# Kernel optimization log

Hardware: AMD Instinct MI355X
Metric: run time of the kernel (lower is better)

## Reference

```python
import jax, jax.numpy as jnp
import numpy as np

B = 32
NUM_CLASSES = 2


def _conv3d(x, w, b):
    # 3x3x3 'same' conv, NCDHW
    y = jax.lax.conv_general_dilated(x, w, (1, 1, 1), [(1, 1)] * 3,
                                     dimension_numbers=("NCDHW", "OIDHW", "NCDHW"))
    return y + b[None, :, None, None, None]


def _bn(x, g, b, axes, eps=1e-5):
    # training-mode batchnorm (biased variance), channel axis = 1
    m = jnp.mean(x, axes, keepdims=True)
    v = jnp.var(x, axes, keepdims=True)
    sh = [1] * x.ndim
    sh[1] = -1
    return (x - m) / jnp.sqrt(v + eps) * g.reshape(sh) + b.reshape(sh)


def _ln(x, g, b, eps=1e-6):
    m = jnp.mean(x, -1, keepdims=True)
    v = jnp.var(x, -1, keepdims=True)
    return (x - m) / jnp.sqrt(v + eps) * g + b


def _lin(x, w, b):
    return x @ w.T + b


def _conv1x1(x, w, b):
    # 1x1x1 Conv3d == channel-mixing linear
    return jnp.einsum("bcdhw,oc->bodhw", x, w) + b[None, :, None, None, None]


def _catnum(t, w, b, g, be, attr, out_attr):
    # Conv1d(attr->196, k=1) == Linear; BN1d over (batch, length); SiLU; tile channels
    t = _lin(t.reshape(t.shape[0], attr), w, b)               # [B,196]
    t = _bn(t[:, :, None], g, be, (0, 2))[:, :, 0]
    t = t * jax.nn.sigmoid(t)                                  # SiLU
    return jnp.broadcast_to(t.reshape(-1, 1, 4, 7, 7), (t.shape[0], out_attr, 4, 7, 7))


def _gcn(t, w, b):
    # all-pairs L1-distance affinity over CHANNELS (detached), then matmul + MLP + residual
    bsz, c = t.shape[0], t.shape[1]
    f = t.reshape(bsz, c, -1)                                  # [B,C,196]
    dist = jax.lax.stop_gradient(
        jnp.exp(-jnp.abs(f[:, :, None, :] - f[:, None, :, :]).sum(-1)))  # [B,C,C]
    out = jax.nn.relu(_lin(jnp.einsum("bij,bjn->bin", dist, f), w, b))
    return out.reshape(t.shape) + t


def _crossatt(img, text, e1_w, e1_b, e2_w, e2_b, f1_w, f1_b, f2_w, f2_b, f3_w, f3_b, f4_w, f4_b):
    # q/k/v each come from the SAME linear applied to the same input -> identical tensors
    iq = jax.nn.relu(_lin(img, e1_w, e1_b))                    # [B,128,196]
    tq = jax.nn.relu(_lin(text, e2_w, e2_b))                   # [B,45,196]
    att = lambda q, k: jax.nn.softmax(jnp.einsum("bik,bjk->bij", q, k), axis=-1)
    img_fea = att(iq, iq) @ iq
    text_fea = att(tq, tq) @ tq
    it_fea = att(iq, tq) @ tq
    ti_fea = att(tq, iq) @ iq
    return (_lin(img_fea, f1_w, f1_b) + _lin(it_fea, f3_w, f3_b) + img,
            _lin(text_fea, f2_w, f2_b) + _lin(ti_fea, f4_w, f4_b) + text)


def _cmsa(xf, w, b, fw, fb):
    # query=key=value (same conv applied thrice to same input)
    bsz, c, d, hh, ww = xf.shape
    q = jax.nn.relu(_conv1x1(xf, w, b)).reshape(bsz, c, -1)    # [B,173,196]
    A = jax.nn.softmax(jnp.einsum("bci,bcj->bij", q, q), axis=-1)  # [B,196,196]
    fea = jnp.einsum("bij,bcj->bci", A, q).reshape(bsz, c, d, hh, ww)
    return jax.nn.relu(_conv1x1(fea, fw, fb)) + xf


def _forward(x, oneHot, num, c1_w1, c1_b1, c1_g1, c1_be1, c1_w2, c1_b2, c1_g2, c1_be2,
             oh_w, oh_b, oh_g, oh_be, nm_w, nm_b, nm_g, nm_be,
             gm1_w, gm1_b, gm2_w, gm2_b, ln1_g, ln1_b, ln2_g, ln2_b,
             e1_w, e1_b, e2_w, e2_b, f1_w, f1_b, f2_w, f2_b, f3_w, f3_b, f4_w, f4_b,
             cm_w, cm_b, cmf_w, cmf_b, cls_w, cls_b):
    h = jax.nn.relu(_bn(_conv3d(x, c1_w1, c1_b1), c1_g1, c1_be1, (0, 2, 3, 4)))
    conv5 = jax.nn.relu(_bn(_conv3d(h, c1_w2, c1_b2), c1_g2, c1_be2, (0, 2, 3, 4)))  # [B,128,4,7,7]
    t_oh = _catnum(oneHot, oh_w, oh_b, oh_g, oh_be, 24, 30)    # [B,30,4,7,7]
    t_nm = _catnum(num, nm_w, nm_b, nm_g, nm_be, 11, 15)       # [B,15,4,7,7]
    text = jnp.concatenate([t_oh, t_nm], axis=1)               # [B,45,4,7,7]
    conv5 = _gcn(conv5, gm1_w, gm1_b)
    text = _gcn(text, gm2_w, gm2_b)
    bsz = x.shape[0]
    c5f = conv5.reshape(bsz, 128, 196)
    txf = text.reshape(bsz, 45, 196)
    ci, ct = _crossatt(_ln(c5f, ln1_g, ln1_b), _ln(txf, ln2_g, ln2_b),
                       e1_w, e1_b, e2_w, e2_b, f1_w, f1_b, f2_w, f2_b, f3_w, f3_b, f4_w, f4_b)
    feat = jnp.concatenate([(ci + c5f).reshape(bsz, 128, 4, 7, 7),
                            (ct + txf).reshape(bsz, 45, 4, 7, 7)], axis=1)  # [B,173,4,7,7]
    cmsa = _cmsa(feat, cm_w, cm_b, cmf_w, cmf_b)
    g1v = t_oh.reshape(bsz, 30, -1).sum(-1)
    g2v = t_nm.reshape(bsz, 15, -1).sum(-1)
    pcm = cmsa.reshape(bsz, 173, -1).sum(-1)
    return _lin(jnp.concatenate([g1v, g2v, pcm], axis=1), cls_w, cls_b)  # [B,num_classes]


def setup_inputs():
    key = jax.random.key(0)
    ks = iter(jax.random.split(key, 64))
    rn = lambda shape, s=0.02: jax.random.normal(next(ks), shape, jnp.float32) * s
    d = {}
    d["x"] = rn((B, 320, 4, 7, 7), 1.0)
    d["oneHot"] = (jax.random.uniform(next(ks), (B, 24)) > 0.5).astype(jnp.float32)
    d["num"] = rn((B, 11), 1.0)
    d["c1_w1"] = rn((128, 320, 3, 3, 3)); d["c1_b1"] = jnp.zeros(128)
    d["c1_g1"] = jnp.ones(128); d["c1_be1"] = jnp.zeros(128)
    d["c1_w2"] = rn((128, 128, 3, 3, 3)); d["c1_b2"] = jnp.zeros(128)
    d["c1_g2"] = jnp.ones(128); d["c1_be2"] = jnp.zeros(128)
    d["oh_w"] = rn((196, 24), 0.1); d["oh_b"] = jnp.zeros(196)
    d["oh_g"] = jnp.ones(196); d["oh_be"] = jnp.zeros(196)
    d["nm_w"] = rn((196, 11), 0.1); d["nm_b"] = jnp.zeros(196)
    d["nm_g"] = jnp.ones(196); d["nm_be"] = jnp.zeros(196)
    d["gm1_w"] = rn((196, 196), 0.05); d["gm1_b"] = jnp.zeros(196)
    d["gm2_w"] = rn((196, 196), 0.05); d["gm2_b"] = jnp.zeros(196)
    d["ln1_g"] = jnp.ones(196); d["ln1_b"] = jnp.zeros(196)
    d["ln2_g"] = jnp.ones(196); d["ln2_b"] = jnp.zeros(196)
    for n in ["e1", "e2", "f1", "f2", "f3", "f4"]:
        d[n + "_w"] = rn((196, 196), 0.05); d[n + "_b"] = jnp.zeros(196)
    d["cm_w"] = rn((173, 173), 0.05); d["cm_b"] = jnp.zeros(173)
    d["cmf_w"] = rn((173, 173), 0.05); d["cmf_b"] = jnp.zeros(173)
    d["cls_w"] = rn((NUM_CLASSES, 218), 0.05); d["cls_b"] = jnp.zeros(NUM_CLASSES)
    return d


def reference(x, oneHot, num, c1_w1, c1_b1, c1_g1, c1_be1, c1_w2, c1_b2, c1_g2, c1_be2,
              oh_w, oh_b, oh_g, oh_be, nm_w, nm_b, nm_g, nm_be,
              gm1_w, gm1_b, gm2_w, gm2_b, ln1_g, ln1_b, ln2_g, ln2_b,
              e1_w, e1_b, e2_w, e2_b, f1_w, f1_b, f2_w, f2_b, f3_w, f3_b, f4_w, f4_b,
              cm_w, cm_b, cmf_w, cmf_b, cls_w, cls_b):
    return _forward(x, oneHot, num, c1_w1, c1_b1, c1_g1, c1_be1, c1_w2, c1_b2, c1_g2, c1_be2,
                    oh_w, oh_b, oh_g, oh_be, nm_w, nm_b, nm_g, nm_be,
                    gm1_w, gm1_b, gm2_w, gm2_b, ln1_g, ln1_b, ln2_g, ln2_b,
                    e1_w, e1_b, e2_w, e2_b, f1_w, f1_b, f2_w, f2_b, f3_w, f3_b, f4_w, f4_b,
                    cm_w, cm_b, cmf_w, cmf_b, cls_w, cls_b)
```

## Files before the change

kernel.cpp:

```cpp
#include <hip/hip_runtime.h>
#include <hip/hip_bf16.h>


using bf16x8 = __attribute__((ext_vector_type(8))) short;
using f32x4  = __attribute__((ext_vector_type(4))) float;

typedef const __attribute__((address_space(1))) void gas_void;
typedef __attribute__((address_space(3))) void las_void;

__device__ __forceinline__ unsigned short f2bf(float f) {
    unsigned int u = __float_as_uint(f);
    u += 0x7FFFu + ((u >> 16) & 1u);
    return (unsigned short)(u >> 16);
}

__device__ __forceinline__ void d_wpack(const float* __restrict__ w,
                                        unsigned short* __restrict__ wp,
                                        int IC, int idx) {
    int nc = IC >> 3;
    if (idx >= 27 * 128 * nc) return;
    int c = idx % nc; int r = idx / nc; int oc = r & 127; int t = r >> 7;
    const float* ws = w + ((size_t)oc * IC + c * 8) * 27 + t;
    unsigned int o0 = f2bf(ws[0])   | ((unsigned int)f2bf(ws[27])  << 16);
    unsigned int o1 = f2bf(ws[54])  | ((unsigned int)f2bf(ws[81])  << 16);
    unsigned int o2 = f2bf(ws[108]) | ((unsigned int)f2bf(ws[135]) << 16);
    unsigned int o3 = f2bf(ws[162]) | ((unsigned int)f2bf(ws[189]) << 16);
    uint4 v; v.x = o0; v.y = o1; v.z = o2; v.w = o3;
    ((uint4*)wp)[idx] = v;
}

__device__ __forceinline__ void d_w173(const float* __restrict__ w,
                                       unsigned short* __restrict__ wb, int idx) {
    if (idx >= 176 * 192) return;
    int oc = idx / 192, c = idx - oc * 192;
    wb[idx] = (oc < 173 && c < 173) ? f2bf(w[(size_t)oc * 173 + c]) : (unsigned short)0;
}

__device__ __forceinline__ void d_wcat(const float* __restrict__ wA,
                                       const float* __restrict__ wB,
                                       unsigned short* __restrict__ outw, int idx) {
    if (idx >= 208 * 448) return;
    int n = idx / 448, k = idx - n * 448;
    unsigned short v = 0;
    if (n < 196) {
        if (k < 196) v = f2bf(wA[(size_t)n * 196 + k]);
        else if (k >= 224 && k < 420) v = f2bf(wB[(size_t)n * 196 + (k - 224)]);
    }
    outw[idx] = v;
}

__device__ __forceinline__ void d_catnum(const float* __restrict__ inp, int A,
                                         const float* __restrict__ w,
                                         const float* __restrict__ bias,
                                         const float* __restrict__ g,
                                         const float* __restrict__ be,
                                         float* __restrict__ outv, int j, int lane) {
    float v = 0.f;
    if (lane < 32) {
        v = bias[j];
        for (int k = 0; k < A; ++k) v += inp[lane * A + k] * w[j * A + k];
    }
    float s = (lane < 32) ? v : 0.f;
    float s2 = (lane < 32) ? v * v : 0.f;
    for (int m = 16; m; m >>= 1) { s += __shfl_xor(s, m, 32); s2 += __shfl_xor(s2, m, 32); }
    if (lane < 32) {
        float mean = s / 32.f;
        float var = s2 / 32.f - mean * mean;
        float rstd = rsqrtf(var + 1e-5f);
        float t = (v - mean) * rstd * g[j] + be[j];
        t = t / (1.f + expf(-t));
        outv[lane * 196 + j] = t;
    }
}

__global__ void k_prep1(const float* __restrict__ c1w1, unsigned short* __restrict__ wp1,
                        const float* __restrict__ c1w2, unsigned short* __restrict__ wp2,
                        const float* __restrict__ x, unsigned short* __restrict__ xt1) {
    int blk = blockIdx.x, tid = threadIdx.x;
    if (blk < 540) { d_wpack(c1w1, wp1, 320, blk * 256 + tid); return; }
    blk -= 540;
    if (blk < 216) { d_wpack(c1w2, wp2, 128, blk * 256 + tid); return; }
    blk -= 216;
    int b = blk / 147, ib = blk - b * 147;
    const int tot = 5 * 208 * 36;
    int idx = ib * 256 + tid;
    if (idx >= tot) return;
    int g = idx / (208 * 36); int r2 = idx - g * (208 * 36);
    int s = r2 / 36, cp = r2 - s * 36;
    int cc = cp * 2;
    int ic = g * 64 + cc;
    unsigned int lo = 0, hi = 0;
    if (s < 196 && cc < 64 && ic < 320)         lo = f2bf(x[((size_t)b * 320 + ic) * 196 + s]);
    if (s < 196 && cc + 1 < 64 && ic + 1 < 320) hi = f2bf(x[((size_t)b * 320 + ic + 1) * 196 + s]);
    ((unsigned int*)xt1)[(size_t)b * tot + idx] = lo | (hi << 16);
}

__global__ void k_prep2(const float* __restrict__ cm_w, unsigned short* __restrict__ wcmb,
                        const float* __restrict__ cmf_w, unsigned short* __restrict__ wcmfb,
                        const float* __restrict__ gm1_w, unsigned short* __restrict__ gm1b,
                        float4* __restrict__ ftbz,
                        const float* __restrict__ gm2_w, const float* __restrict__ e1_w,
                        const float* __restrict__ e2_w, float* __restrict__ wT) {
    int blk = blockIdx.x, tid = threadIdx.x;
    if (blk < 132) { d_w173(cm_w, wcmb, blk * 256 + tid); return; }
    blk -= 132;
    if (blk < 132) { d_w173(cmf_w, wcmfb, blk * 256 + tid); return; }
    blk -= 132;
    if (blk < 182) {
        int idx = blk * 256 + tid;
        if (idx < 208 * 224) {
            int r = idx / 224, c = idx - r * 224;
            gm1b[idx] = (r < 196 && c < 196) ? f2bf(gm1_w[(size_t)r * 196 + c])
                                             : (unsigned short)0;
        }
        return;
    }
    blk -= 182;
    if (blk < 624) {
        int i = blk * 256 + tid;
        if (i < 159744) ftbz[i] = (float4){0.f, 0.f, 0.f, 0.f};
        return;
    }
    blk -= 624;
    {
        int m = blk / 196, i = blk - m * 196;
        const float* w = (m == 0) ? gm2_w : (m == 1) ? e1_w : e2_w;
        float* o = wT + (size_t)m * 38416;
        if (tid < 196) o[(size_t)i * 196 + tid] = w[(size_t)tid * 196 + i];
    }
}

__global__ void k_catnum2(const float* __restrict__ oneHot, const float* __restrict__ num,
                          const float* __restrict__ ohw, const float* __restrict__ ohb,
                          const float* __restrict__ ohg, const float* __restrict__ ohbe,
                          const float* __restrict__ nmw, const float* __restrict__ nmb,
                          const float* __restrict__ nmg, const float* __restrict__ nmbe,
                          float* __restrict__ toh, float* __restrict__ tnm) {
    int blk = blockIdx.x;
    if (blk < 196) d_catnum(oneHot, 24, ohw, ohb, ohg, ohbe, toh, blk, threadIdx.x);
    else           d_catnum(num, 11, nmw, nmb, nmg, nmbe, tnm, blk - 196, threadIdx.x);
}

__device__ __forceinline__ void d_dist_img(const float* __restrict__ f,
                                           const float* __restrict__ fT,
                                           unsigned short* __restrict__ distb,
                                           int bx, int b, int tid) {
    __shared__ float fi[4][196];
    const int i0 = bx * 4;
    for (int idx = tid; idx < 4 * 196; idx += 256) {
        int r = idx / 196, n = idx - r * 196;
        fi[r][n] = f[((size_t)(b * 128 + i0 + r)) * 196 + n];
    }
    __syncthreads();
    if (tid < 128) {
        const float* ft = fT + (size_t)b * 196 * 128 + tid;
        float a[4];
#pragma unroll
        for (int r = 0; r < 4; ++r) a[r] = 0.f;
#pragma unroll 4
        for (int n = 0; n < 196; ++n) {
            float v = ft[(size_t)n * 128];
#pragma unroll
            for (int r = 0; r < 4; ++r) a[r] += fabsf(fi[r][n] - v);
        }
#pragma unroll
        for (int r = 0; r < 4; ++r)
            distb[((size_t)(b * 128 + i0 + r)) * 128 + tid] = f2bf(expf(-a[r]));
    }
}

__device__ __forceinline__ void d_dist_txt(const float* __restrict__ f,
                                           const float* __restrict__ fT,
                                           float* __restrict__ dist,
// ... 327 lines not shown
                    int col = nt * 16 + a;
                    p0[((size_t)b * 208 + row) * 224 + col] = f2bf(e[nt] * inv);
                }
            }
        }
    } else if (EPI == 2) {
#pragma unroll
        for (int nt = 0; nt < 13; ++nt) {
            if (nt < NT0 || nt >= NT0 + NTN) continue;
            int col = nt * 16 + a;
#pragma unroll
            for (int j = 0; j < 4; ++j) {
                int row = mbase + j;
                if (row < 173)
                    p0[((size_t)b * 208 + col) * 192 + row] = f2bf(acc[nt][j]);
            }
        }
    } else if (EPI == 3) {
#pragma unroll
        for (int nt = 0; nt < 13; ++nt) {
            if (nt < NT0 || nt >= NT0 + NTN) continue;
            int col = nt * 16 + a;
            if (col < 196) {
#pragma unroll
                for (int j = 0; j < 4; ++j) {
                    int row = mbase + j;
                    if (row < 173) {
                        size_t rr = ((size_t)b * 173 + row) * 196 + col;
                        outf[rr] = fmaxf(acc[nt][j] + bias[row], 0.f) + resid[rr];
                    }
                }
            }
        }
    } else if (EPI == 7) {
#pragma unroll
        for (int nt = 0; nt < 13; ++nt) {
            if (nt < NT0 || nt >= NT0 + NTN) continue;
            int col = nt * 16 + a;
#pragma unroll
            for (int j = 0; j < 4; ++j) {
                int row = mbase + j;
                unsigned short h = (col < 196) ? f2bf(acc[nt][j]) : (unsigned short)0;
                p0[((size_t)b * 128 + row) * 224 + col] = h;
            }
        }
    } else {
#pragma unroll
        for (int nt = 0; nt < 13; ++nt) {
            if (nt < NT0 || nt >= NT0 + NTN) continue;
            int col = nt * 16 + a;
            if (col < 196) {
#pragma unroll
                for (int j = 0; j < 4; ++j) {
                    int row = mbase + j;
                    size_t rr = ((size_t)b * 128 + row) * 196 + col;
                    outf[rr] = fmaxf(acc[nt][j] + bias[col], 0.f) + resid[rr];
                }
            }
        }
    }
}

template <int MROWS, int MTILES, int KPA, int KPB, int KK, int EPI, int STAGEA, int NS>
__global__ __launch_bounds__(256, 2) void k_agemm(
    const unsigned short* __restrict__ Ab, size_t ABS,
    const unsigned short* __restrict__ Bb, size_t BBS,
    const float* __restrict__ biasA, const float* __restrict__ biasB,
    const float* __restrict__ lnres, const float* __restrict__ res2,
    unsigned short* __restrict__ p0, size_t p0rs, size_t p0bs,
    float* __restrict__ feat, unsigned short* __restrict__ ftb, int cbase) {
    constexpr int KPS = KPA + 8;
    __shared__ unsigned short xsA[STAGEA ? 64 * KPS : 64];
    __shared__ char bbuf[2][208 * 64];
    const int tid = threadIdx.x, bx = blockIdx.x, b = blockIdx.y;
    const int wv = tid >> 6, lane = tid & 63, a = lane & 15, kg = lane >> 4;
    const int nh = bx % NS, mg = bx / NS;
    const int NT0 = (NS == 1) ? 0 : nh * 7;
    const int NTN = (NS == 1) ? 13 : ((nh == 0) ? 7 : 6);

    const unsigned short* Abase = Ab + (size_t)b * ABS;
    if (STAGEA) {
        const int rowu = KPA / 2;
        for (int i = tid; i < 64 * rowu; i += 256) {
            int r = i / rowu, cu = i - r * rowu;
            int gr = mg * 64 + r; if (gr > MROWS - 1) gr = MROWS - 1;
            unsigned int v = ((const unsigned int*)(Abase + (size_t)gr * KPA))[cu];
            *(unsigned int*)&xsA[r * KPS + cu * 2] = v;
        }
    }
    const char* Bbase = (const char*)(Bb + (size_t)b * BBS);
    auto stageB = [&](int kk) {
        char* dst0 = &bbuf[kk & 1][0];
        const int cnt = NTN * 64;
#pragma unroll
        for (int c = 0; c < 4; ++c) {
            int idx = tid + c * 256;
            if (idx < cnt) {
                int lrow = idx >> 2, u = idx & 3;
                int grow = NT0 * 16 + lrow;
                gas_void* src = (gas_void*)(Bbase + (size_t)grow * (KPB * 2) +
                                            kk * 64 + u * 16);
                __builtin_amdgcn_global_load_lds(src, (las_void*)(dst0 + (size_t)idx * 16),
                                                 16, 0, 0);
            }
        }
    };

    int mt = mg * 4 + wv; if (mt > MTILES - 1) mt = MTILES - 1;

    f32x4 acc[13];
#pragma unroll
    for (int nt = 0; nt < 13; ++nt) acc[nt] = (f32x4){0.f, 0.f, 0.f, 0.f};

    stageB(0);
    __syncthreads();
    for (int kk = 0; kk < KK; ++kk) {
        if (kk + 1 < KK) stageB(kk + 1);
        bf16x8 Af;
        if (STAGEA) {
            int arow = mt * 16 + a - mg * 64;
            Af = *(const bf16x8*)&xsA[arow * KPS + kk * 32 + kg * 8];
        } else {
            int gr = mt * 16 + a; if (gr > MROWS - 1) gr = MROWS - 1;
// ... 19 lines not shown
#pragma unroll
            for (int nt = 0; nt < 8; ++nt) mA = fmaxf(mA, acc[nt][j]);
#pragma unroll
            for (int nt = 8; nt < 13; ++nt) {
                int col = nt * 16 + a;
                float s = (col < 173) ? acc[nt][j] : -3.4e38f;
                mB = fmaxf(mB, s);
            }
            for (int msk = 1; msk < 16; msk <<= 1) {
                mA = fmaxf(mA, __shfl_xor(mA, msk));
                mB = fmaxf(mB, __shfl_xor(mB, msk));
            }
            float eA[8], eB[5];
            float sA = 0.f, sB = 0.f;
#pragma unroll
            for (int nt = 0; nt < 8; ++nt) { eA[nt] = expf(acc[nt][j] - mA); sA += eA[nt]; }
#pragma unroll
            for (int nt = 8; nt < 13; ++nt) {
                int col = nt * 16 + a;
                float v = (col < 173) ? expf(acc[nt][j] - mB) : 0.f;
                eB[nt - 8] = v; sB += v;
            }
            for (int msk = 1; msk < 16; msk <<= 1) {
                sA += __shfl_xor(sA, msk);
                sB += __shfl_xor(sB, msk);
            }
            float iA = 1.f / sA, iB = 1.f / sB;
            if (row < MROWS) {
#pragma unroll
                for (int nt = 0; nt < 12; ++nt) {
                    int col = nt * 16 + a;
                    float v = (nt < 8) ? eA[nt] * iA
                                       : ((col < 173) ? eB[nt - 8] * iB : 0.f);
                    p0[(size_t)b * p0bs + (size_t)row * p0rs + col] = f2bf(v);
                }
            }
        }
    } else {
#pragma unroll
        for (int nt = 0; nt < 13; ++nt) {
            if (nt < NT0 || nt >= NT0 + NTN) continue;
            int col = nt * 16 + a;
            if (col < 196) {
#pragma unroll
                for (int j = 0; j < 4; ++j) {
                    int row = mbase + j;
                    if (row < MROWS) {
                        size_t rr = ((size_t)b * MROWS + row) * 196 + col;
                        float v = acc[nt][j] + biasA[col] + biasB[col] +
                                  lnres[rr] + res2[rr];
                        feat[((size_t)b * 173 + cbase + row) * 196 + col] = v;
                        ftb[((size_t)(b * 208 + col)) * 192 + cbase + row] = f2bf(v);
                    }
                }
            }
        }
    }
}

template <int MROWS, int MTILES, int NS>
__global__ __launch_bounds__(256, 2) void k_pv(
    const unsigned short* __restrict__ P, size_t Pbs,
    const unsigned short* __restrict__ V1, size_t V1bs,
    const unsigned short* __restrict__ V2, size_t V2bs,
    unsigned short* __restrict__ F, size_t Fbs) {
    constexpr int KPS = 200;
    __shared__ unsigned short xsA[64 * KPS];
    __shared__ char bbuf[2][208 * 64];
    const int tid = threadIdx.x, bx = blockIdx.x, b = blockIdx.y;
    const int wv = tid >> 6, lane = tid & 63, a = lane & 15, kg = lane >> 4;
    const int nh = bx % NS, mg = bx / NS;
    const int NT0 = (NS == 1) ? 0 : nh * 7;
    const int NTN = (NS == 1) ? 13 : ((nh == 0) ? 7 : 6);

    const unsigned short* Abase = P + (size_t)b * Pbs;
    {
        for (int i = tid; i < 64 * 96; i += 256) {
            int r = i / 96, cu = i - r * 96;
            int gr = mg * 64 + r; if (gr > MROWS - 1) gr = MROWS - 1;
            unsigned int v = ((const unsigned int*)(Abase + (size_t)gr * 192))[cu];
            *(unsigned int*)&xsA[r * KPS + cu * 2] = v;
        }
    }
    int mt = mg * 4 + wv; if (mt > MTILES - 1) mt = MTILES - 1;
    const int arow = mt * 16 + a - mg * 64;
    const int mbase = mt * 16 + kg * 4;

    auto run = [&](const unsigned short* Vb, size_t Vbs_, int KPB, int KK,
                   int AOFFe, int outoff) {
        f32x4 acc[13];
#pragma unroll
        for (int nt = 0; nt < 13; ++nt) acc[nt] = (f32x4){0.f, 0.f, 0.f, 0.f};
        const char* Bbase = (const char*)(Vb + (size_t)b * Vbs_);
        auto stageB = [&](int kk) {
            char* dst0 = &bbuf[kk & 1][0];
            const int cnt = NTN * 64;
#pragma unroll
            for (int c = 0; c < 4; ++c) {
                int idx = tid + c * 256;
                if (idx < cnt) {
                    int lrow = idx >> 2, u = idx & 3;
                    int grow = NT0 * 16 + lrow;
                    gas_void* src = (gas_void*)(Bbase + (size_t)grow * (KPB * 2) +
                                                kk * 64 + u * 16);
                    __builtin_amdgcn_global_load_lds(src,
                        (las_void*)(dst0 + (size_t)idx * 16), 16, 0, 0);
                }
            }
        };
        stageB(0);
        __syncthreads();
        for (int kk = 0; kk < KK; ++kk) {
            if (kk + 1 < KK) stageB(kk + 1);
            bf16x8 Af = *(const bf16x8*)&xsA[arow * KPS + AOFFe + kk * 32 + kg * 8];
            const char* bb = &bbuf[kk & 1][0];
#pragma unroll
            for (int nt = 0; nt < 13; ++nt) {
                if (nt >= NT0 && nt < NT0 + NTN) {
                    bf16x8 Bf = *(const bf16x8*)(bb + ((nt - NT0) * 16 + a) * 64 + kg * 16);
                    acc[nt] = __builtin_amdgcn_mfma_f32_16x16x32_bf16(Af, Bf, acc[nt], 0, 0, 0);
                }
            }
            __syncthreads();
        }
#pragma unroll
        for (int nt = 0; nt < 13; ++nt) {
            if (nt < NT0 || nt >= NT0 + NTN) continue;
            int col = nt * 16 + a;
#pragma unroll
            for (int j = 0; j < 4; ++j) {
                int row = mbase + j;
                if (row < MROWS) {
                    unsigned short h = (col < 196) ? f2bf(acc[nt][j]) : (unsigned short)0;
                    F[(size_t)b * Fbs + (size_t)row * 448 + outoff + col] = h;
                }
            }
        }
        if (nh == NS - 1) {
            int col = 208 + a;
#pragma unroll
            for (int j = 0; j < 4; ++j) {
                int row = mbase + j;
                if (row < MROWS)
                    F[(size_t)b * Fbs + (size_t)row * 448 + outoff + col] = 0;
            }
        }
    };
    run(V1, V1bs, 128, 4, 0, 0);
    run(V2, V2bs, 64, 2, 128, 224);
}

template <int C, int ROWS>
__global__ void k_gcn_spmmfin_t(const float* __restrict__ dist, const float* __restrict__ f,
                                const float* __restrict__ wt, const float* __restrict__ bias,
                                float* __restrict__ outp) {
    __shared__ float ds[ROWS][C];
    __shared__ float ts[ROWS][196];
    const int i0 = blockIdx.x * ROWS, b = blockIdx.y;
    const int tid = threadIdx.x;
    for (int idx = tid; idx < ROWS * C; idx += 256) {
        int r = idx / C, j = idx - r * C;
        ds[r][j] = dist[((size_t)(b * C + i0 + r)) * C + j];
    }
    __syncthreads();
    if (tid < 196) {
        float a[ROWS];
#pragma unroll
        for (int r = 0; r < ROWS; ++r) a[r] = 0.f;
#pragma unroll 4
        for (int j = 0; j < C; ++j) {
            float v = f[((size_t)b * C + j) * 196 + tid];
#pragma unroll
            for (int r = 0; r < ROWS; ++r) a[r] += ds[r][j] * v;
        }
#pragma unroll
        for (int r = 0; r < ROWS; ++r) ts[r][tid] = a[r];
    }
    __syncthreads();
    if (tid < 196) {
        float a[ROWS];
        float bi = bias[tid];
#pragma unroll
        for (int r = 0; r < ROWS; ++r) a[r] = bi;
#pragma unroll 4
        for (int n = 0; n < 196; ++n) {
            float wv = wt[(size_t)n * 196 + tid];
#pragma unroll
            for (int r = 0; r < ROWS; ++r) a[r] += ts[r][n] * wv;
        }
#pragma unroll
        for (int r = 0; r < ROWS; ++r) {
            size_t rr = ((size_t)(b * C + i0 + r)) * 196 + tid;
            outp[rr] = fmaxf(a[r], 0.f) + f[rr];
        }
    }
}

__global__ void k_textbuild(const float* __restrict__ toh, const float* __restrict__ tnm,
                            float* __restrict__ text, float* __restrict__ textT) {
    int idx = blockIdx.x;
    int b = idx / 45, c = idx - b * 45;
    int s = threadIdx.x;
    if (s < 196) {
        float v = (c < 30) ? toh[b * 196 + s] : tnm[b * 196 + s];
        text[(size_t)idx * 196 + s] = v;
        textT[((size_t)b * 196 + s) * 45 + c] = v;
    }
}

template <int R, int ROWS, int KOFF, int TS>
__device__ __forceinline__ void d_lnlin(const float* __restrict__ x,
                                        const float* __restrict__ g,
                                        const float* __restrict__ be,
                                        const float* __restrict__ eT,
                                        const float* __restrict__ eb,
                                        float* __restrict__ lnout,
                                        unsigned short* __restrict__ kcat,
                                        unsigned short* __restrict__ tbuf,
                                        int bx, int b) {
    __shared__ float ls[ROWS][196];
    const int i0 = bx * ROWS;
    const int tid = threadIdx.x;
    const int wv = tid >> 6, lane = tid & 63;
    for (int idx = tid; idx < ROWS * 196; idx += 256) {
        int r = idx / 196, n = idx - r * 196;
        ls[r][n] = x[((size_t)(b * R + i0 + r)) * 196 + n];
    }
    __syncthreads();
    for (int k = 0;; ++k) {
        int r = wv + 4 * k;
        if (r >= ROWS) break;
        float s = 0.f, s2 = 0.f;
        for (int j = lane; j < 196; j += 64) { float v = ls[r][j]; s += v; s2 += v * v; }
        for (int sh = 32; sh; sh >>= 1) { s += __shfl_xor(s, sh); s2 += __shfl_xor(s2, sh); }
        float mean = s / 196.f;
        float var = s2 / 196.f - mean * mean;
        float rstd = rsqrtf(var + 1e-6f);
        size_t rowo = ((size_t)(b * R + i0 + r)) * 196;
        for (int j = lane; j < 196; j += 64) {
            float l = (ls[r][j] - mean) * rstd * g[j] + be[j];
// ... 102 lines not shown
    const float* gm2_w  = (const float*)d_in[21];
    const float* gm2_b  = (const float*)d_in[22];
    const float* ln1_g  = (const float*)d_in[23];
    const float* ln1_b  = (const float*)d_in[24];
    const float* ln2_g  = (const float*)d_in[25];
    const float* ln2_b  = (const float*)d_in[26];
    const float* e1_w   = (const float*)d_in[27];
    const float* e1_b   = (const float*)d_in[28];
    const float* e2_w   = (const float*)d_in[29];
    const float* e2_b   = (const float*)d_in[30];
    const float* f1_w   = (const float*)d_in[31];
    const float* f1_b   = (const float*)d_in[32];
    const float* f2_w   = (const float*)d_in[33];
    const float* f2_b   = (const float*)d_in[34];
    const float* f3_w   = (const float*)d_in[35];
    const float* f3_b   = (const float*)d_in[36];
    const float* f4_w   = (const float*)d_in[37];
    const float* f4_b   = (const float*)d_in[38];
    const float* cm_w   = (const float*)d_in[39];
    const float* cm_b   = (const float*)d_in[40];
    const float* cmf_w  = (const float*)d_in[41];
    const float* cmf_b  = (const float*)d_in[42];
    const float* cls_w  = (const float*)d_in[43];
    const float* cls_b  = (const float*)d_in[44];
    float* out = (float*)d_out;
    float* W = (float*)d_ws;

    const size_t L = 802816;
    const size_t T = 282240;
    const size_t F3 = 1085056;
    const size_t o_A    = 0;
    const size_t o_B    = L;
    const size_t o_C    = 2 * L;
    const size_t o_part = 3 * L;
    const size_t o_Kcat = 3 * L;
    const size_t o_iqT  = o_Kcat + 745472;
    const size_t o_t1   = 4 * L + T;
    const size_t o_t3   = 4 * L + 2 * T;
    const size_t o_ln2  = 4 * L + 3 * T;
    const size_t o_toh  = 4 * L + 4 * T;
    const size_t o_tnm  = o_toh + 6272;
    const size_t o_st   = o_tnm + 6272;
    const size_t o_wT   = o_st + 1024;
    const size_t o_feat = o_wT + 8 * 38416;
    const size_t o_q    = o_feat + F3;
    const size_t o_Fimg = o_q;
    const size_t o_dd   = o_q + F3;
    const size_t o_db   = o_dd;
    const size_t o_d2   = o_dd + 524288;
    const size_t o_gm1b = o_dd + 589088;
    const size_t o_fTb  = o_dd + 612384;
    const size_t o_tqT  = o_dd;
    const size_t o_wcI  = o_dd + 212992;
    const size_t o_wcT  = o_wcI + 46592;
    const size_t o_pbf  = o_dd;
    const size_t o_rs   = o_dd;
    const size_t o_qbf  = o_dd + 745472;
    const size_t o_Ftxt = o_qbf;
    const size_t o_wcm  = o_qbf + 630784;
    const size_t o_wcmf = o_wcm + 16896;
    const size_t o_ftb  = o_wcmf + 16896;
    const size_t o_tr   = o_ftb + 638976;
    const size_t o_Pimg = o_tr;
    const size_t o_Ptxt = o_tr + 393216;
    const size_t o_qtb  = o_tr;
    const size_t o_feab = o_qtb + 638976;
    const size_t o_ps   = 10158208;
    const size_t o_xt1 = o_dd;
    const size_t o_xt2 = o_xt1 + 1198080;
    const size_t o_wp1 = o_xt2 + 479232;
    const size_t o_wp2 = o_wp1 + 552960;

    float* part = W + o_part;
    unsigned short* xt1 = (unsigned short*)(W + o_xt1);
    unsigned short* xt2 = (unsigned short*)(W + o_xt2);
    unsigned short* wp1 = (unsigned short*)(W + o_wp1);
    unsigned short* wp2 = (unsigned short*)(W + o_wp2);
    unsigned short* kcatb = (unsigned short*)(W + o_Kcat);
    unsigned short* iqTb = (unsigned short*)(W + o_iqT);
    unsigned short* tqTb = (unsigned short*)(W + o_tqT);
    unsigned short* wcatI = (unsigned short*)(W + o_wcI);
    unsigned short* wcatT = (unsigned short*)(W + o_wcT);
    unsigned short* Fimg = (unsigned short*)(W + o_Fimg);
    unsigned short* Ftxt = (unsigned short*)(W + o_Ftxt);
    unsigned short* Pimg = (unsigned short*)(W + o_Pimg);
    unsigned short* Ptxt = (unsigned short*)(W + o_Ptxt);
    unsigned short* ftb = (unsigned short*)(W + o_ftb);
    unsigned short* qtb = (unsigned short*)(W + o_qtb);
    unsigned short* feab = (unsigned short*)(W + o_feab);
    unsigned short* qbf = (unsigned short*)(W + o_qbf);
    unsigned short* wcmb = (unsigned short*)(W + o_wcm);
    unsigned short* wcmfb = (unsigned short*)(W + o_wcmf);
    unsigned short* pbf = (unsigned short*)(W + o_pbf);
    unsigned short* distb = (unsigned short*)(W + o_db);
    unsigned short* gm1b = (unsigned short*)(W + o_gm1b);
    unsigned short* fTb = (unsigned short*)(W + o_fTb);
    unsigned short* tmpb = (unsigned short*)(W + o_A);
    float* gm2T = W + o_wT + 0 * 38416;
    float* e1T  = W + o_wT + 1 * 38416;
    float* e2T  = W + o_wT + 2 * 38416;

    k_prep1<<<5460, 256, 0, stream>>>(c1_w1, wp1, c1_w2, wp2, x, xt1);

    k_convchunk4<320, 5, 4, 2><<<dim3(20, 32), 256, 0, stream>>>(xt1, wp1, part);
    k_reduce_stats<5, 128><<<dim3(128, 32), 256, 0, stream>>>(part, W + o_A, W + o_ps);
    k_bn_apply2<<<4096, 256, 0, stream>>>(W + o_A, W + o_ps, c1_g1, c1_be1,
                                          nullptr, nullptr, xt2, 128);

    k_convchunk4<128, 2, 2, 4><<<dim3(16, 32), 256, 0, stream>>>(xt2, wp2, part);
    k_reduce_stats<2, 128><<<dim3(128, 32), 256, 0, stream>>>(part, W + o_B,
                                                              W + o_ps + 8192);
    k_bn_apply2<<<4096, 256, 0, stream>>>(W + o_B, W + o_ps + 8192, c1_g2, c1_be2,
                                          W + o_tr, fTb, nullptr, 128);

    k_prep2<<<1658, 256, 0, stream>>>(cm_w, wcmb, cmf_w, wcmfb, gm1_w, gm1b,
                                      (float4*)(W + o_ftb), gm2_w, e1_w, e2_w, W + o_wT);

    k_catnum2<<<392, 64, 0, stream>>>(oneHot, num, oh_w, oh_b, oh_g, oh_be,
                                      nm_w, nm_b, nm_g, nm_be, W + o_toh, W + o_tnm);
    k_textbuild<<<32 * 45, 256, 0, stream>>>(W + o_toh, W + o_tnm, W + o_t1, W + o_tr + L);

    k_dist_both<<<1504, 256, 0, stream>>>(W + o_B, W + o_tr, distb,
                                          W + o_t1, W + o_tr + L, W + o_d2);

    k_bgemm<128, 8, 128, 4, 7, 2><<<dim3(4, 32), 256, 0, stream>>>(
        distb, (size_t)128 * 128, fTb, (size_t)208 * 128, nullptr,
        tmpb, nullptr, nullptr, nullptr);
    k_bgemm<128, 8, 224, 7, 8, 2><<<dim3(4, 32), 256, 0, stream>>>(
        tmpb, (size_t)128 * 224, gm1b, 0, gm1_b,
        nullptr, nullptr, W + o_B, W + o_C);

    k_gcn_spmmfin_t<45, 3><<<dim3(15, 32), 256, 0, stream>>>(W + o_d2, W + o_t1, gm2T,
                                                             gm2_b, W + o_t3);

    k_prep3<<<936, 256, 0, stream>>>((float4*)(W + o_tqT), f1_w, f3_w, wcatI,
                                     f4_w, f2_w, wcatT);

    k_lnlin_both<<<1504, 256, 0, stream>>>(W + o_C, ln1_g, ln1_b, e1T, e1_b, W + o_B,
                                           W + o_t3, ln2_g, ln2_b, e2T, e2_b, W + o_ln2,
                                           kcatb, iqTb, tqTb);

    k_agemm<128, 8, 224, 224, 7, 5, 1, 1><<<dim3(2, 32), 256, 0, stream>>>(
        kcatb, (size_t)208 * 224, kcatb, (size_t)208 * 224,
        nullptr, nullptr, nullptr, nullptr, Pimg, 192, (size_t)128 * 192,
        nullptr, nullptr, 0);
    k_agemm<45, 3, 224, 224, 7, 5, 1, 1><<<dim3(1, 32), 256, 0, stream>>>(
        kcatb + 128 * 224, (size_t)208 * 224, kcatb, (size_t)208 * 224,
        nullptr, nullptr, nullptr, nullptr, Ptxt, 192, (size_t)48 * 192,
        nullptr, nullptr, 0);

    k_pv<128, 8, 2><<<dim3(4, 32), 256, 0, stream>>>(
        Pimg, (size_t)128 * 192, iqTb, (size_t)208 * 128, tqTb, (size_t)208 * 64,
        Fimg, (size_t)128 * 448);
    k_pv<45, 3, 2><<<dim3(2, 32), 256, 0, stream>>>(
        Ptxt, (size_t)48 * 192, iqTb, (size_t)208 * 128, tqTb, (size_t)208 * 64,
        Ftxt, (size_t)48 * 448);

    k_agemm<128, 8, 448, 448, 14, 4, 0, 2><<<dim3(4, 32), 256, 0, stream>>>(
        Fimg, (size_t)128 * 448, wcatI, 0,
        f1_b, f3_b, W + o_B, W + o_C, nullptr, 0, 0, W + o_feat, ftb, 0);
    k_agemm<45, 3, 448, 448, 14, 4, 0, 2><<<dim3(2, 32), 256, 0, stream>>>(
        Ftxt, (size_t)48 * 448, wcatT, 0,
        f2_b, f4_b, W + o_ln2, W + o_t3, nullptr, 0, 0, W + o_feat, ftb, 128);

    k_prep4<<<2592, 256, 0, stream>>>((float4*)(W + o_pbf), (float4*)(W + o_qtb));

    k_bgemm<176, 11, 192, 6, 0, 2><<<dim3(6, 32), 256, 0, stream>>>(
        wcmb, 0, ftb, (size_t)208 * 192, cm_b, qbf, qtb, nullptr, nullptr);
    k_bgemm<208, 13, 192, 6, 1, 1><<<dim3(4, 32), 256, 0, stream>>>(
        qtb, (size_t)208 * 192, qtb, (size_t)208 * 192, nullptr, pbf, nullptr,
        nullptr, nullptr);
    k_bgemm<176, 11, 224, 7, 2, 2><<<dim3(6, 32), 256, 0, stream>>>(
        qbf, (size_t)176 * 224, pbf, (size_t)208 * 224, nullptr, feab, nullptr,
        nullptr, nullptr);
    k_bgemm<176, 11, 192, 6, 3, 2><<<dim3(6, 32), 256, 0, stream>>>(
        wcmfb, 0, feab, (size_t)208 * 192, cmf_b, nullptr, nullptr,
        W + o_feat, W + o_q);

    k_finale<<<32, 256, 0, stream>>>(W + o_toh, W + o_tnm, W + o_q, cls_w, cls_b, out);
}
```

Baseline: 369.9 us.

## Merge paired image/text kernels into single launches to cut launch count

Several launches are merged. The catnum BN/SiLU kernel now writes the tiled text tensor and its transpose directly, removing the separate textbuild kernel. The dist×f MFMA GEMM and the text GCN spmm/MLP now run as one kernel whose blocks branch by blockIdx. The image and text attention GEMMs, PV and fusion GEMMs are each combined into one launch using parameter structs and a block split index. This removes about six launches and their serial gaps, and lets small text work share the grid with image work. The cost is some runtime parameter selection, MROWS/MTILES turned from compile-time template values into runtime values, and a larger shared-memory footprint from the union in the fused kernel.

```diff
diff --git a/kernel.cpp b/kernel.cpp
--- a/kernel.cpp
+++ b/kernel.cpp
@@ -47,30 +47,6 @@
         else if (k >= 224 && k < 420) v = f2bf(wB[(size_t)n * 196 + (k - 224)]);
     }
     outw[idx] = v;
-}
-
-__device__ __forceinline__ void d_catnum(const float* __restrict__ inp, int A,
-                                         const float* __restrict__ w,
-                                         const float* __restrict__ bias,
-                                         const float* __restrict__ g,
-                                         const float* __restrict__ be,
-                                         float* __restrict__ outv, int j, int lane) {
-    float v = 0.f;
-    if (lane < 32) {
-        v = bias[j];
-        for (int k = 0; k < A; ++k) v += inp[lane * A + k] * w[j * A + k];
-    }
-    float s = (lane < 32) ? v : 0.f;
-    float s2 = (lane < 32) ? v * v : 0.f;
-    for (int m = 16; m; m >>= 1) { s += __shfl_xor(s, m, 32); s2 += __shfl_xor(s2, m, 32); }
-    if (lane < 32) {
-        float mean = s / 32.f;
-        float var = s2 / 32.f - mean * mean;
-        float rstd = rsqrtf(var + 1e-5f);
-        float t = (v - mean) * rstd * g[j] + be[j];
-        t = t / (1.f + expf(-t));
-        outv[lane * 196 + j] = t;
-    }
 }
 
 __global__ void k_prep1(const float* __restrict__ c1w1, unsigned short* __restrict__ wp1,
@@ -130,15 +106,52 @@
     }
 }
 
-__global__ void k_catnum2(const float* __restrict__ oneHot, const float* __restrict__ num,
+__global__ void k_cattext(const float* __restrict__ oneHot, const float* __restrict__ num,
                           const float* __restrict__ ohw, const float* __restrict__ ohb,
                           const float* __restrict__ ohg, const float* __restrict__ ohbe,
                           const float* __restrict__ nmw, const float* __restrict__ nmb,
                           const float* __restrict__ nmg, const float* __restrict__ nmbe,
-                          float* __restrict__ toh, float* __restrict__ tnm) {
+                          float* __restrict__ toh, float* __restrict__ tnm,
+                          float* __restrict__ text, float* __restrict__ textT) {
     int blk = blockIdx.x;
-    if (blk < 196) d_catnum(oneHot, 24, ohw, ohb, ohg, ohbe, toh, blk, threadIdx.x);
-    else           d_catnum(num, 11, nmw, nmb, nmg, nmbe, tnm, blk - 196, threadIdx.x);
+    int lane = threadIdx.x;
+    const int isOH = (blk < 196);
+    const int j = isOH ? blk : blk - 196;
+    const float* inp = isOH ? oneHot : num;
+    const int A = isOH ? 24 : 11;
+    const float* w = isOH ? ohw : nmw;
+    const float* bias = isOH ? ohb : nmb;
+    const float* g = isOH ? ohg : nmg;
+    const float* be = isOH ? ohbe : nmbe;
+    float v = 0.f;
+    if (lane < 32) {
+        v = bias[j];
+        for (int k = 0; k < A; ++k) v += inp[lane * A + k] * w[j * A + k];
+    }
+    float s = (lane < 32) ? v : 0.f;
+    float s2 = (lane < 32) ? v * v : 0.f;
+    for (int m = 16; m; m >>= 1) { s += __shfl_xor(s, m, 32); s2 += __shfl_xor(s2, m, 32); }
+    if (lane < 32) {
+        float mean = s / 32.f;
+        float var = s2 / 32.f - mean * mean;
+        float rstd = rsqrtf(var + 1e-5f);
+        float t = (v - mean) * rstd * g[j] + be[j];
+        t = t / (1.f + expf(-t));
+        int b = lane;
+        if (isOH) {
+            toh[b * 196 + j] = t;
+            for (int c = 0; c < 30; ++c) {
+                text[((size_t)(b * 45 + c)) * 196 + j] = t;
+                textT[((size_t)(b * 196 + j)) * 45 + c] = t;
+            }
+        } else {
+            tnm[b * 196 + j] = t;
+            for (int c = 30; c < 45; ++c) {
+                text[((size_t)(b * 45 + c)) * 196 + j] = t;
+                textT[((size_t)(b * 196 + j)) * 45 + c] = t;
+            }
+        }
+    }
 }
 
 __device__ __forceinline__ void d_dist_img(const float* __restrict__ f,
@@ -532,18 +545,6 @@
                 }
             }
         }
-    } else if (EPI == 7) {
-#pragma unroll
-        for (int nt = 0; nt < 13; ++nt) {
-            if (nt < NT0 || nt >= NT0 + NTN) continue;
-            int col = nt * 16 + a;
-#pragma unroll
-            for (int j = 0; j < 4; ++j) {
-                int row = mbase + j;
-                unsigned short h = (col < 196) ? f2bf(acc[nt][j]) : (unsigned short)0;
-                p0[((size_t)b * 128 + row) * 224 + col] = h;
-            }
-        }
     } else {
 #pragma unroll
         for (int nt = 0; nt < 13; ++nt) {
@@ -561,24 +562,144 @@
     }
 }
 
-template <int MROWS, int MTILES, int KPA, int KPB, int KK, int EPI, int STAGEA, int NS>
-__global__ __launch_bounds__(256, 2) void k_agemm(
-    const unsigned short* __restrict__ Ab, size_t ABS,
-    const unsigned short* __restrict__ Bb, size_t BBS,
-    const float* __restrict__ biasA, const float* __restrict__ biasB,
-    const float* __restrict__ lnres, const float* __restrict__ res2,
-    unsigned short* __restrict__ p0, size_t p0rs, size_t p0bs,
-    float* __restrict__ feat, unsigned short* __restrict__ ftb, int cbase) {
+__global__ __launch_bounds__(256, 2) void k_gcnpair(
+    const unsigned short* __restrict__ distb, const unsigned short* __restrict__ fTb,
+    unsigned short* __restrict__ tmpb,
+    const float* __restrict__ d2, const float* __restrict__ t1,
+    const float* __restrict__ gm2T, const float* __restrict__ gm2b,
+    float* __restrict__ t3) {
+    __shared__ unsigned short xsA[64 * 136];
+    __shared__ char bbuf[2][208 * 64];
+    __shared__ float ds[3][45];
+    __shared__ float ts[3][196];
+    const int tid = threadIdx.x, b = blockIdx.y;
+    int bx = blockIdx.x;
+    if (bx < 4) {
+        const int wv = tid >> 6, lane = tid & 63, a = lane & 15, kg = lane >> 4;
+        const int nh = bx % 2, mg = bx / 2;
+        const int NT0 = nh * 7, NTN = (nh == 0) ? 7 : 6;
+        const unsigned short* Abase = distb + (size_t)b * 128 * 128;
+        for (int i = tid; i < 64 * 64; i += 256) {
+            int r = i / 64, cu = i - r * 64;
+            int gr = mg * 64 + r;
+            unsigned int v = ((const unsigned int*)(Abase + (size_t)gr * 128))[cu];
+            *(unsigned int*)&xsA[r * 136 + cu * 2] = v;
+        }
+        const char* Bbase = (const char*)(fTb + (size_t)b * 208 * 128);
+        auto stageB = [&](int kk) {
+            char* dst0 = &bbuf[kk & 1][0];
+            const int cnt = NTN * 64;
+#pragma unroll
+            for (int c = 0; c < 4; ++c) {
+                int idx = tid + c * 256;
+                if (idx < cnt) {
+                    int lrow = idx >> 2, u = idx & 3;
+                    int grow = NT0 * 16 + lrow;
+                    gas_void* src = (gas_void*)(Bbase + (size_t)grow * 256 +
+                                                kk * 64 + u * 16);
+                    __builtin_amdgcn_global_load_lds(src,
+                        (las_void*)(dst0 + (size_t)idx * 16), 16, 0, 0);
+                }
+            }
+        };
+        int mt = mg * 4 + wv;
+        const int arow = mt * 16 + a - mg * 64;
+        f32x4 acc[13];
+#pragma unroll
+        for (int nt = 0; nt < 13; ++nt) acc[nt] = (f32x4){0.f, 0.f, 0.f, 0.f};
+        stageB(0);
+        __syncthreads();
+        for (int kk = 0; kk < 4; ++kk) {
+            if (kk + 1 < 4) stageB(kk + 1);
+            bf16x8 Af = *(const bf16x8*)&xsA[arow * 136 + kk * 32 + kg * 8];
+            const char* bb = &bbuf[kk & 1][0];
+#pragma unroll
+            for (int nt = 0; nt < 13; ++nt) {
+                if (nt >= NT0 && nt < NT0 + NTN) {
+                    bf16x8 Bf = *(const bf16x8*)(bb + ((nt - NT0) * 16 + a) * 64 + kg * 16);
+                    acc[nt] = __builtin_amdgcn_mfma_f32_16x16x32_bf16(Af, Bf, acc[nt], 0, 0, 0);
+                }
+            }
+            __syncthreads();
+        }
+        const int mbase = mt * 16 + kg * 4;
+#pragma unroll
+        for (int nt = 0; nt < 13; ++nt) {
+            if (nt < NT0 || nt >= NT0 + NTN) continue;
+            int col = nt * 16 + a;
+#pragma unroll
+            for (int j = 0; j < 4; ++j) {
+                int row = mbase + j;
+                unsigned short h = (col < 196) ? f2bf(acc[nt][j]) : (unsigned short)0;
+                tmpb[((size_t)b * 128 + row) * 224 + col] = h;
+            }
+        }
+    } else {
+        const int i0 = (bx - 4) * 3;
+        for (int idx = tid; idx < 3 * 45; idx += 256) {
+            int r = idx / 45, j = idx - r * 45;
+            ds[r][j] = d2[((size_t)(b * 45 + i0 + r)) * 45 + j];
+        }
+        __syncthreads();
+        if (tid < 196) {
+            float a[3];
+#pragma unroll
+            for (int r = 0; r < 3; ++r) a[r] = 0.f;
+#pragma unroll 4
+            for (int j = 0; j < 45; ++j) {
+                float v = t1[((size_t)b * 45 + j) * 196 + tid];
+#pragma unroll
+                for (int r = 0; r < 3; ++r) a[r] += ds[r][j] * v;
+            }
+#pragma unroll
+            for (int r = 0; r < 3; ++r) ts[r][tid] = a[r];
+        }
+        __syncthreads();
+        if (tid < 196) {
+            float a[3];
+            float bi = gm2b[tid];
+#pragma unroll
+            for (int r = 0; r < 3; ++r) a[r] = bi;
+#pragma unroll 4
+            for (int n = 0; n < 196; ++n) {
+                float wv = gm2T[(size_t)n * 196 + tid];
+#pragma unroll
+                for (int r = 0; r < 3; ++r) a[r] += ts[r][n] * wv;
+            }
+#pragma unroll
+            for (int r = 0; r < 3; ++r) {
+                size_t rr = ((size_t)(b * 45 + i0 + r)) * 196 + tid;
+                t3[rr] = fmaxf(a[r], 0.f) + t1[rr];
+            }
+        }
+    }
+}
+
+struct AG {
+    const unsigned short* Ab; unsigned long ABS;
+    const unsigned short* Bb; unsigned long BBS;
+    const float* biasA; const float* biasB;
+    const float* lnres; const float* res2;
+    unsigned short* p0; unsigned long p0rs, p0bs;
+    float* feat; unsigned short* ftb; int cbase;
+    int MROWS; int MTILES;
+};
+
+template <int KPA, int KPB, int KK, int EPI, int STAGEA, int NS>
+__global__ __launch_bounds__(256, 2) void k_agemm2(AG pa, AG pc, int split) {
     constexpr int KPS = KPA + 8;
     __shared__ unsigned short xsA[STAGEA ? 64 * KPS : 64];
     __shared__ char bbuf[2][208 * 64];
-    const int tid = threadIdx.x, bx = blockIdx.x, b = blockIdx.y;
+    const AG P = (blockIdx.x < split) ? pa : pc;
+    const int bx = (blockIdx.x < split) ? blockIdx.x : blockIdx.x - split;
+    const int tid = threadIdx.x, b = blockIdx.y;
     const int wv = tid >> 6, lane = tid & 63, a = lane & 15, kg = lane >> 4;
     const int nh = bx % NS, mg = bx / NS;
     const int NT0 = (NS == 1) ? 0 : nh * 7;
     const int NTN = (NS == 1) ? 13 : ((nh == 0) ? 7 : 6);
-
-    const unsigned short* Abase = Ab + (size_t)b * ABS;
+    const int MROWS = P.MROWS, MTILES = P.MTILES;
+
+    const unsigned short* Abase = P.Ab + (size_t)b * P.ABS;
     if (STAGEA) {
         const int rowu = KPA / 2;
         for (int i = tid; i < 64 * rowu; i += 256) {
@@ -588,7 +709,7 @@
             *(unsigned int*)&xsA[r * KPS + cu * 2] = v;
         }
     }
-    const char* Bbase = (const char*)(Bb + (size_t)b * BBS);
+    const char* Bbase = (const char*)(P.Bb + (size_t)b * P.BBS);
     auto stageB = [&](int kk) {
         char* dst0 = &bbuf[kk & 1][0];
         const int cnt = NTN * 64;
@@ -674,7 +795,7 @@
                     int col = nt * 16 + a;
                     float v = (nt < 8) ? eA[nt] * iA
                                        : ((col < 173) ? eB[nt - 8] * iB : 0.f);
-                    p0[(size_t)b * p0bs + (size_t)row * p0rs + col] = f2bf(v);
+                    P.p0[(size_t)b * P.p0bs + (size_t)row * P.p0rs + col] = f2bf(v);
                 }
             }
         }
@@ -689,10 +810,10 @@
                     int row = mbase + j;
                     if (row < MROWS) {
                         size_t rr = ((size_t)b * MROWS + row) * 196 + col;
-                        float v = acc[nt][j] + biasA[col] + biasB[col] +
-                                  lnres[rr] + res2[rr];
-                        feat[((size_t)b * 173 + cbase + row) * 196 + col] = v;
-                        ftb[((size_t)(b * 208 + col)) * 192 + cbase + row] = f2bf(v);
+                        float v = acc[nt][j] + P.biasA[col] + P.biasB[col] +
+                                  P.lnres[rr] + P.res2[rr];
+                        P.feat[((size_t)b * 173 + P.cbase + row) * 196 + col] = v;
+                        P.ftb[((size_t)(b * 208 + col)) * 192 + P.cbase + row] = f2bf(v);
                     }
                 }
             }
@@ -700,22 +821,25 @@
     }
 }
 
-template <int MROWS, int MTILES, int NS>
-__global__ __launch_bounds__(256, 2) void k_pv(
-    const unsigned short* __restrict__ P, size_t Pbs,
-    const unsigned short* __restrict__ V1, size_t V1bs,
-    const unsigned short* __restrict__ V2, size_t V2bs,
-    unsigned short* __restrict__ F, size_t Fbs) {
+struct PVP { const unsigned short* P; unsigned long Pbs;
+             unsigned short* F; unsigned long Fbs; int MROWS; int MTILES; };
+
+__global__ __launch_bounds__(256, 2) void k_pv2(
+    PVP pa, PVP pc, int split,
+    const unsigned short* __restrict__ V1, unsigned long V1bs,
+    const unsigned short* __restrict__ V2, unsigned long V2bs) {
     constexpr int KPS = 200;
     __shared__ unsigned short xsA[64 * KPS];
     __shared__ char bbuf[2][208 * 64];
-    const int tid = threadIdx.x, bx = blockIdx.x, b = blockIdx.y;
+    const PVP P = (blockIdx.x < split) ? pa : pc;
+    const int bx = (blockIdx.x < split) ? blockIdx.x : blockIdx.x - split;
+    const int tid = threadIdx.x, b = blockIdx.y;
     const int wv = tid >> 6, lane = tid & 63, a = lane & 15, kg = lane >> 4;
-    const int nh = bx % NS, mg = bx / NS;
-    const int NT0 = (NS == 1) ? 0 : nh * 7;
-    const int NTN = (NS == 1) ? 13 : ((nh == 0) ? 7 : 6);
-
-    const unsigned short* Abase = P + (size_t)b * Pbs;
+    const int nh = bx % 2, mg = bx / 2;
+    const int NT0 = nh * 7, NTN = (nh == 0) ? 7 : 6;
+    const int MROWS = P.MROWS, MTILES = P.MTILES;
+
+    const unsigned short* Abase = P.P + (size_t)b * P.Pbs;
     {
         for (int i = tid; i < 64 * 96; i += 256) {
             int r = i / 96, cu = i - r * 96;
@@ -774,80 +898,22 @@
                 int row = mbase + j;
                 if (row < MROWS) {
                     unsigned short h = (col < 196) ? f2bf(acc[nt][j]) : (unsigned short)0;
-                    F[(size_t)b * Fbs + (size_t)row * 448 + outoff + col] = h;
+                    P.F[(size_t)b * P.Fbs + (size_t)row * 448 + outoff + col] = h;
                 }
             }
         }
-        if (nh == NS - 1) {
+        if (nh == 1) {
             int col = 208 + a;
 #pragma unroll
             for (int j = 0; j < 4; ++j) {
                 int row = mbase + j;
                 if (row < MROWS)
-                    F[(size_t)b * Fbs + (size_t)row * 448 + outoff + col] = 0;
+                    P.F[(size_t)b * P.Fbs + (size_t)row * 448 + outoff + col] = 0;
             }
         }
     };
     run(V1, V1bs, 128, 4, 0, 0);
     run(V2, V2bs, 64, 2, 128, 224);
-}
-
-template <int C, int ROWS>
-__global__ void k_gcn_spmmfin_t(const float* __restrict__ dist, const float* __restrict__ f,
-                                const float* __restrict__ wt, const float* __restrict__ bias,
-                                float* __restrict__ outp) {
-    __shared__ float ds[ROWS][C];
-    __shared__ float ts[ROWS][196];
-    const int i0 = blockIdx.x * ROWS, b = blockIdx.y;
-    const int tid = threadIdx.x;
-    for (int idx = tid; idx < ROWS * C; idx += 256) {
-        int r = idx / C, j = idx - r * C;
-        ds[r][j] = dist[((size_t)(b * C + i0 + r)) * C + j];
-    }
-    __syncthreads();
-    if (tid < 196) {
-        float a[ROWS];
-#pragma unroll
-        for (int r = 0; r < ROWS; ++r) a[r] = 0.f;
-#pragma unroll 4
-        for (int j = 0; j < C; ++j) {
-            float v = f[((size_t)b * C + j) * 196 + tid];
-#pragma unroll
-            for (int r = 0; r < ROWS; ++r) a[r] += ds[r][j] * v;
-        }
-#pragma unroll
-        for (int r = 0; r < ROWS; ++r) ts[r][tid] = a[r];
-    }
-    __syncthreads();
-    if (tid < 196) {
-        float a[ROWS];
-        float bi = bias[tid];
-#pragma unroll
-        for (int r = 0; r < ROWS; ++r) a[r] = bi;
-#pragma unroll 4
-        for (int n = 0; n < 196; ++n) {
-            float wv = wt[(size_t)n * 196 + tid];
-#pragma unroll
-            for (int r = 0; r < ROWS; ++r) a[r] += ts[r][n] * wv;
-        }
-#pragma unroll
-        for (int r = 0; r < ROWS; ++r) {
-            size_t rr = ((size_t)(b * C + i0 + r)) * 196 + tid;
-            outp[rr] = fmaxf(a[r], 0.f) + f[rr];
-        }
-    }
-}
-
-__global__ void k_textbuild(const float* __restrict__ toh, const float* __restrict__ tnm,
-                            float* __restrict__ text, float* __restrict__ textT) {
-    int idx = blockIdx.x;
-    int b = idx / 45, c = idx - b * 45;
-    int s = threadIdx.x;
-    if (s < 196) {
-        float v = (c < 30) ? toh[b * 196 + s] : tnm[b * 196 + s];
-        text[(size_t)idx * 196 + s] = v;
-        textT[((size_t)b * 196 + s) * 45 + c] = v;
-    }
 }
 
 template <int R, int ROWS, int KOFF, int TS>
@@ -1016,7 +1082,6 @@
     const size_t o_A    = 0;
     const size_t o_B    = L;
     const size_t o_C    = 2 * L;
-    const size_t o_part = 3 * L;
     const size_t o_Kcat = 3 * L;
     const size_t o_iqT  = o_Kcat + 745472;
     const size_t o_t1   = 4 * L + T;
@@ -1038,7 +1103,6 @@
     const size_t o_wcI  = o_dd + 212992;
     const size_t o_wcT  = o_wcI + 46592;
     const size_t o_pbf  = o_dd;
-    const size_t o_rs   = o_dd;
     const size_t o_qbf  = o_dd + 745472;
     const size_t o_Ftxt = o_qbf;
     const size_t o_wcm  = o_qbf + 630784;
@@ -1048,14 +1112,13 @@
     const size_t o_Pimg = o_tr;
     const size_t o_Ptxt = o_tr + 393216;
     const size_t o_qtb  = o_tr;
-    const size_t o_feab = o_qtb + 638976;
     const size_t o_ps   = 10158208;
     const size_t o_xt1 = o_dd;
     const size_t o_xt2 = o_xt1 + 1198080;
     const size_t o_wp1 = o_xt2 + 479232;
     const size_t o_wp2 = o_wp1 + 552960;
 
-    float* part = W + o_part;
+    float* part = W + 3 * L;
     unsigned short* xt1 = (unsigned short*)(W + o_xt1);
     unsigned short* xt2 = (unsigned short*)(W + o_xt2);
     unsigned short* wp1 = (unsigned short*)(W + o_wp1);
@@ -1071,7 +1134,7 @@
     unsigned short* Ptxt = (unsigned short*)(W + o_Ptxt);
     unsigned short* ftb = (unsigned short*)(W + o_ftb);
     unsigned short* qtb = (unsigned short*)(W + o_qtb);
-    unsigned short* feab = (unsigned short*)(W + o_feab);
+    unsigned short* feab = (unsigned short*)(W + o_qtb + 638976);
     unsigned short* qbf = (unsigned short*)(W + o_qbf);
     unsigned short* wcmb = (unsigned short*)(W + o_wcm);
     unsigned short* wcmfb = (unsigned short*)(W + o_wcmf);
@@ -1100,23 +1163,21 @@
     k_prep2<<<1658, 256, 0, stream>>>(cm_w, wcmb, cmf_w, wcmfb, gm1_w, gm1b,
                                       (float4*)(W + o_ftb), gm2_w, e1_w, e2_w, W + o_wT);
 
-    k_catnum2<<<392, 64, 0, stream>>>(oneHot, num, oh_w, oh_b, oh_g, oh_be,
-                                      nm_w, nm_b, nm_g, nm_be, W + o_toh, W + o_tnm);
-    k_textbuild<<<32 * 45, 256, 0, stream>>>(W + o_toh, W + o_tnm, W + o_t1, W + o_tr + L);
+    k_cattext<<<392, 64, 0, stream>>>(oneHot, num, oh_w, oh_b, oh_g, oh_be,
+                                      nm_w, nm_b, nm_g, nm_be,
+                                      W + o_toh, W + o_tnm, W + o_t1, W + o_tr + L);
 
     k_dist_both<<<1504, 256, 0, stream>>>(W + o_B, W + o_tr, distb,
                                           W + o_t1, W + o_tr + L, W + o_d2);
 
-    k_bgemm<128, 8, 128, 4, 7, 2><<<dim3(4, 32), 256, 0, stream>>>(
-        distb, (size_t)128 * 128, fTb, (size_t)208 * 128, nullptr,
-        tmpb, nullptr, nullptr, nullptr);
+    k_gcnpair<<<dim3(19, 32), 256, 0, stream>>>(distb, fTb, tmpb,
+                                                W + o_d2, W + o_t1, gm2T, gm2_b,
+                                                W + o_t3);
+
     k_bgemm<128, 8, 224, 7, 8, 2><<<dim3(4, 32), 256, 0, stream>>>(
         tmpb, (size_t)128 * 224, gm1b, 0, gm1_b,
         nullptr, nullptr, W + o_B, W + o_C);
 
-    k_gcn_spmmfin_t<45, 3><<<dim3(15, 32), 256, 0, stream>>>(W + o_d2, W + o_t1, gm2T,
-                                                             gm2_b, W + o_t3);
-
     k_prep3<<<936, 256, 0, stream>>>((float4*)(W + o_tqT), f1_w, f3_w, wcatI,
                                      f4_w, f2_w, wcatT);
 
@@ -1124,28 +1185,35 @@
                                            W + o_t3, ln2_g, ln2_b, e2T, e2_b, W + o_ln2,
                                            kcatb, iqTb, tqTb);
 
-    k_agemm<128, 8, 224, 224, 7, 5, 1, 1><<<dim3(2, 32), 256, 0, stream>>>(
-        kcatb, (size_t)208 * 224, kcatb, (size_t)208 * 224,
-        nullptr, nullptr, nullptr, nullptr, Pimg, 192, (size_t)128 * 192,
-        nullptr, nullptr, 0);
-    k_agemm<45, 3, 224, 224, 7, 5, 1, 1><<<dim3(1, 32), 256, 0, stream>>>(
-        kcatb + 128 * 224, (size_t)208 * 224, kcatb, (size_t)208 * 224,
-        nullptr, nullptr, nullptr, nullptr, Ptxt, 192, (size_t)48 * 192,
-        nullptr, nullptr, 0);
-
-    k_pv<128, 8, 2><<<dim3(4, 32), 256, 0, stream>>>(
-        Pimg, (size_t)128 * 192, iqTb, (size_t)208 * 128, tqTb, (size_t)208 * 64,
-        Fimg, (size_t)128 * 448);
-    k_pv<45, 3, 2><<<dim3(2, 32), 256, 0, stream>>>(
-        Ptxt, (size_t)48 * 192, iqTb, (size_t)208 * 128, tqTb, (size_t)208 * 64,
-        Ftxt, (size_t)48 * 448);
-
-    k_agemm<128, 8, 448, 448, 14, 4, 0, 2><<<dim3(4, 32), 256, 0, stream>>>(
-        Fimg, (size_t)128 * 448, wcatI, 0,
-        f1_b, f3_b, W + o_B, W + o_C, nullptr, 0, 0, W + o_feat, ftb, 0);
-    k_agemm<45, 3, 448, 448, 14, 4, 0, 2><<<dim3(2, 32), 256, 0, stream>>>(
-        Ftxt, (size_t)48 * 448, wcatT, 0,
-        f2_b, f4_b, W + o_ln2, W + o_t3, nullptr, 0, 0, W + o_feat, ftb, 128);
+    {
+        AG a{}, c{};
+        a.Ab = kcatb; a.ABS = 208 * 224; a.Bb = kcatb; a.BBS = 208 * 224;
+        a.p0 = Pimg; a.p0rs = 192; a.p0bs = (unsigned long)128 * 192;
+        a.MROWS = 128; a.MTILES = 8;
+        c = a;
+        c.Ab = kcatb + 128 * 224; c.p0 = Ptxt; c.p0bs = (unsigned long)48 * 192;
+        c.MROWS = 45; c.MTILES = 3;
+        k_agemm2<224, 224, 7, 5, 1, 1><<<dim3(3, 32), 256, 0, stream>>>(a, c, 2);
+    }
+
+    {
+        PVP a{Pimg, (unsigned long)128 * 192, Fimg, (unsigned long)128 * 448, 128, 8};
+        PVP c{Ptxt, (unsigned long)48 * 192, Ftxt, (unsigned long)48 * 448, 45, 3};
+        k_pv2<<<dim3(6, 32), 256, 0, stream>>>(a, c, 4, iqTb, (unsigned long)208 * 128,
+                                               tqTb, (unsigned long)208 * 64);
+    }
+
+    {
+        AG a{}, c{};
+        a.Ab = Fimg; a.ABS = (unsigned long)128 * 448; a.Bb = wcatI; a.BBS = 0;
+        a.biasA = f1_b; a.biasB = f3_b; a.lnres = W + o_B; a.res2 = W + o_C;
+        a.feat = W + o_feat; a.ftb = ftb; a.cbase = 0; a.MROWS = 128; a.MTILES = 8;
+        c = a;
+        c.Ab = Ftxt; c.ABS = (unsigned long)48 * 448; c.Bb = wcatT;
+        c.biasA = f2_b; c.biasB = f4_b; c.lnres = W + o_ln2; c.res2 = W + o_t3;
+        c.cbase = 128; c.MROWS = 45; c.MTILES = 3;
+        k_agemm2<448, 448, 14, 4, 0, 2><<<dim3(6, 32), 256, 0, stream>>>(a, c, 4);
+    }
 
     k_prep4<<<2592, 256, 0, stream>>>((float4*)(W + o_pbf), (float4*)(W + o_qtb));
 
```

Measured after the change: 317.9 us. 1.16x faster.
